# Performance work log

Measured on AMD Instinct MI355X. Metric: run time of the kernel, lower is better.

Reference implementation:

```python
import jax, jax.numpy as jnp
import numpy as np

N_NODES = 4096
N_EDGES = 524288
IN_DIM = 6
EMB_N = 4
EMB_D = 8
EDGE_D = 1
HID = 64
N_HEADS = 4
LN_EPS = 1e-5


def _layernorm(h, g, b):
    m = jnp.mean(h, axis=-1, keepdims=True)
    v = jnp.mean(jnp.square(h - m), axis=-1, keepdims=True)
    return (h - m) * jax.lax.rsqrt(v + LN_EPS) * g + b


def setup_inputs() -> dict:
    key = jax.random.key(0)
    ks = jax.random.split(key, 16)
    s = lambda fan_in: 1.0 / np.sqrt(fan_in)
    inp = {
        'x': jax.random.normal(ks[0], (N_NODES, IN_DIM), jnp.float32),
        'edge_attr': jax.random.uniform(ks[1], (N_EDGES, EDGE_D), jnp.float32),
        'entity_emb': jax.random.normal(ks[2], (EMB_N, EMB_D), jnp.float32),
        'lin1_w': jax.random.uniform(ks[3], (HID, IN_DIM + EMB_D + EDGE_D), jnp.float32, -s(15), s(15)),
        'lin1_b': jnp.zeros((HID,), jnp.float32),
        'lay_w': jax.random.uniform(ks[4], (HID, HID), jnp.float32, -s(HID), s(HID)),
        'lay_b': jnp.zeros((HID,), jnp.float32),
        'ln_g': jnp.ones((HID,), jnp.float32),
        'ln_b': jnp.zeros((HID,), jnp.float32),
        'in_proj_w': jax.random.uniform(ks[5], (3 * HID, HID), jnp.float32, -s(HID), s(HID)),
        'in_proj_b': jnp.zeros((3 * HID,), jnp.float32),
        'out_proj_w': jax.random.uniform(ks[6], (HID, HID), jnp.float32, -s(HID), s(HID)),
        'out_proj_b': jnp.zeros((HID,), jnp.float32),
        'an_g': jnp.ones((HID,), jnp.float32),
        'an_b': jnp.zeros((HID,), jnp.float32),
        'out_w': jax.random.uniform(ks[7], (HID, HID), jnp.float32, -s(HID), s(HID)),
        'out_b': jnp.zeros((HID,), jnp.float32),
        'edge_index': jax.random.randint(ks[8], (2, N_EDGES), 0, N_NODES, jnp.int64),
        'entity_type': jax.random.randint(ks[9], (N_NODES,), 0, EMB_N, jnp.int64),
    }
    return inp


def reference(x, edge_attr, entity_emb, lin1_w, lin1_b, lay_w, lay_b, ln_g, ln_b,
              in_proj_w, in_proj_b, out_proj_w, out_proj_b, an_g, an_b, out_w, out_b,
              edge_index, entity_type):
    # --- EmbedConv ---
    # concat node features with entity embedding: [N, 6+8]
    xe = jnp.concatenate([x, entity_emb[entity_type]], axis=-1)
    src, dst = edge_index[0], edge_index[1]
    # gather source nodes + edge attr: [E, 15]
    msg = jnp.concatenate([xe[src], edge_attr], axis=-1)
    msg = _layernorm(jax.nn.relu(msg @ lin1_w.T + lin1_b), ln_g, ln_b)
    # layer_N = 1 extra layer, shared LayerNorm
    msg = _layernorm(jax.nn.relu(msg @ lay_w.T + lay_b), ln_g, ln_b)
    # scatter-add aggregate into destination nodes: [N, 64]
    h = jax.ops.segment_sum(msg, dst, num_segments=N_NODES)
    # --- MultiheadAttention over all nodes as one sequence (eval: no dropout) ---
    qkv = h @ in_proj_w.T + in_proj_b  # [N, 3H]
    q, k, v = jnp.split(qkv, 3, axis=-1)
    hd = HID // N_HEADS
    q = q.reshape(N_NODES, N_HEADS, hd).transpose(1, 0, 2)  # [h, n, d]
    k = k.reshape(N_NODES, N_HEADS, hd).transpose(1, 0, 2)
    v = v.reshape(N_NODES, N_HEADS, hd).transpose(1, 0, 2)
    scores = jnp.einsum('hnd,hmd->hnm', q, k) / np.sqrt(hd)
    attn = jax.nn.softmax(scores, axis=-1)
    o = jnp.einsum('hnm,hmd->hnd', attn, v).transpose(1, 0, 2).reshape(N_NODES, HID)
    o = o @ out_proj_w.T + out_proj_b
    h = _layernorm(h + o, an_g, an_b)
    # --- output layer ---
    return h @ out_w.T + out_b
```

## Files before the change

### kernel.cpp

```cpp
#include <hip/hip_runtime.h>

#define N_NODES 4096
#define N_EDGES 524288
#define HID 64

typedef short short8 __attribute__((ext_vector_type(8)));
typedef float f32x4 __attribute__((ext_vector_type(4)));
typedef float f32x16 __attribute__((ext_vector_type(16)));

__device__ __forceinline__ float bcastf(float v, int l) {
    return __int_as_float(__builtin_amdgcn_readlane(__float_as_int(v), l));
}

__device__ __forceinline__ void wave_sum2(float& a, float& b) {
    #pragma unroll
    for (int off = 32; off > 0; off >>= 1) {
        a += __shfl_xor(a, off, 64);
        b += __shfl_xor(b, off, 64);
    }
}

__device__ __forceinline__ short f2bf(float f) {
    unsigned u = __float_as_uint(f);
    u = u + 0x7FFFu + ((u >> 16) & 1u);
    return (short)(u >> 16);
}
__device__ __forceinline__ float bf2f(short s) {
    return __uint_as_float(((unsigned)(unsigned short)s) << 16);
}
__device__ __forceinline__ void split_cheap(float f, short& hi, short& lo) {
    unsigned u = __float_as_uint(f);
    unsigned hb = u & 0xffff0000u;
    float lof = f - __uint_as_float(hb);
    hi = (short)(u >> 16);
    lo = (short)(__float_as_uint(lof) >> 16);
}

__global__ void hist_prep(const float* __restrict__ x, const float* __restrict__ emb,
                          const int* __restrict__ etype, const int* __restrict__ ei,
                          const float* __restrict__ w1, const float* __restrict__ b1,
                          const float* __restrict__ w2, const float* __restrict__ lng,
                          const float* __restrict__ lnb, const float* __restrict__ b2,
                          const float* __restrict__ ipw,
                          float* __restrict__ A1, int* __restrict__ cnt, int* __restrict__ rank,
                          unsigned short* __restrict__ w2fh, unsigned short* __restrict__ w2fl,
                          unsigned short* __restrict__ ipfh, unsigned short* __restrict__ ipfl,
                          float* __restrict__ b2p) {
    int tid = blockIdx.x * 256 + threadIdx.x;
    int d = ei[N_EDGES + tid];
    rank[tid] = atomicAdd(&cnt[d], 1);
    if (tid < N_NODES * 64) {
        int n = tid >> 6, f = tid & 63;
        const float* wr = w1 + f * 15;
        float acc = b1[f];
        #pragma unroll
        for (int k = 0; k < 6; k++) acc = fmaf(x[n * 6 + k], wr[k], acc);
        int e = etype[n];
        #pragma unroll
        for (int k = 0; k < 8; k++) acc = fmaf(emb[e * 8 + k], wr[6 + k], acc);
        A1[tid] = acc;
    }
    if (tid < 4096) {
        int idx = tid >> 9, ln = (tid >> 3) & 63, j = tid & 7;
        int mm = ln & 15, qq = ln >> 4;
        int g = idx >> 1, tt = idx & 1;
        int col = tt * 32 + qq * 8 + j;
        float w = w2[(g * 16 + mm) * 64 + col] * lng[col];
        short hi = f2bf(w);
        w2fh[tid] = (unsigned short)hi;
        w2fl[tid] = (unsigned short)f2bf(w - bf2f(hi));
    }
    if (tid < 12288) {
        int idx = tid >> 9, ln = (tid >> 3) & 63, j = tid & 7;
        int mm = ln & 15, qq = ln >> 4;
        int og = idx >> 1, tt = idx & 1;
        float w = ipw[(og * 16 + mm) * 64 + tt * 32 + qq * 8 + j];
        short hi = f2bf(w);
        ipfh[tid] = (unsigned short)hi;
        ipfl[tid] = (unsigned short)f2bf(w - bf2f(hi));
    }
    if (tid < 64) {
        float acc = b2[tid];
        for (int c = 0; c < 64; c++) acc = fmaf(w2[tid * 64 + c], lnb[c], acc);
        b2p[tid] = acc;
    }
}

__global__ void __launch_bounds__(256) scatter_scan(
        const int* __restrict__ cnt, const int* __restrict__ ei,
        const float* __restrict__ edge_attr, const int* __restrict__ rank,
        int* __restrict__ bnd,
        int* __restrict__ ssrc, float* __restrict__ sea) {
    __shared__ int lbnd[4096];
    __shared__ int wsum[4];
    int t = threadIdx.x;
    int base = t * 16;
    int v16[16];
    int T = 0;
    #pragma unroll
    for (int j = 0; j < 16; j++) { v16[j] = cnt[base + j]; T += v16[j]; }
    int inc = T;
    int l = t & 63;
    #pragma unroll
    for (int off = 1; off < 64; off <<= 1) {
        int v = __shfl_up(inc, off, 64);
        if (l >= off) inc += v;
    }
    if (l == 63) wsum[t >> 6] = inc;
    __syncthreads();
    int wo = 0;
    for (int w = 0; w < (t >> 6); w++) wo += wsum[w];
    int run = wo + inc - T;
    #pragma unroll
    for (int j = 0; j < 16; j++) {
        lbnd[base + j] = run;
        run += v16[j];
    }
    if (blockIdx.x == 0) {
        #pragma unroll
        for (int j = 0; j < 16; j++) bnd[base + j] = lbnd[base + j];
        if (t == 255) bnd[4096] = run;
    }
    __syncthreads();
    int e = blockIdx.x * 256 + t;
    int d = ei[N_EDGES + e];
    int pos = lbnd[d] + rank[e];
    ssrc[pos] = ei[e];
    sea[pos] = edge_attr[e];
}

__global__ void __launch_bounds__(256, 4) edge_gather_mfma(
        const float* __restrict__ A1,
        const int* __restrict__ ssrc, const float* __restrict__ sea,
        const int* __restrict__ bnd,
        const unsigned short* __restrict__ w2fh, const unsigned short* __restrict__ w2fl,
        const float* __restrict__ w1, const float* __restrict__ b2p,
        const float* __restrict__ lg, const float* __restrict__ lb,
        float* __restrict__ h) {
    __shared__ uint4 lw2h4[512];
    __shared__ uint4 lw2l4[512];
    __shared__ float hpart[4][64];
    int tid = threadIdx.x;
    {
        const uint4* gh = (const uint4*)w2fh;
        const uint4* gl = (const uint4*)w2fl;
        lw2h4[tid] = gh[tid];
        lw2h4[tid + 256] = gh[tid + 256];
        lw2l4[tid] = gl[tid];
        lw2l4[tid + 256] = gl[tid + 256];
    }
    const unsigned short* lw2h = (const unsigned short*)lw2h4;
    const unsigned short* lw2l = (const unsigned short*)lw2l4;

    int lane = tid & 63;
    int wv = tid >> 6;
    int m = lane & 15;
    int q = lane >> 4;

    float w14f[16];
    #pragma unroll
    for (int t2 = 0; t2 < 2; t2++)
        #pragma unroll
        for (int j = 0; j < 8; j++)
            w14f[t2 * 8 + j] = w1[(t2 * 32 + q * 8 + j) * 15 + 14];
    float b2v[4];
    #pragma unroll
    for (int g = 0; g < 4; g++) b2v[g] = b2p[g * 16 + m];

    int node = blockIdx.x;
    int start = bnd[node], end = bnd[node + 1];
    int ntiles = (end - start + 15) >> 4;
    float acc[4] = {0.f, 0.f, 0.f, 0.f};
    __syncthreads();

    for (int t = wv; t < ntiles; t += 4) {
        int base = start + t * 16;
        int e = base + m;
        int ec = (e < end) ? e : (end - 1);
        int srcn = ssrc[ec];
        float eav = sea[ec];
        const float* ar = A1 + srcn * 64 + q * 8;
        float4 va = *(const float4*)(ar);
        float4 vb = *(const float4*)(ar + 4);
        float4 vc = *(const float4*)(ar + 32);
        float4 vd = *(const float4*)(ar + 36);
        float v[16] = {va.x, va.y, va.z, va.w, vb.x, vb.y, vb.z, vb.w,
                       vc.x, vc.y, vc.z, vc.w, vd.x, vd.y, vd.z, vd.w};
        float s = 0.f, s2 = 0.f;
        #pragma unroll
        for (int j = 0; j < 16; j++) {
            float u = fmaxf(fmaf(w14f[j], eav, v[j]), 0.f);
            v[j] = u;
            s += u;
            s2 = fmaf(u, u, s2);
        }
        s += __shfl_xor(s, 16, 64);  s2 += __shfl_xor(s2, 16, 64);
        s += __shfl_xor(s, 32, 64);  s2 += __shfl_xor(s2, 32, 64);
        float mean = s * (1.f / 64.f);
        float var = s2 * (1.f / 64.f) - mean * mean;
        float rs = rsqrtf(var + 1e-5f);
        float a0 = -mean * rs;
        short8 a2h[2], a2l[2];
        #pragma unroll
        for (int t2 = 0; t2 < 2; t2++)
            #pragma unroll
            for (int j = 0; j < 8; j++) {
                short hi, lo;
                split_cheap(fmaf(v[t2 * 8 + j], rs, a0), hi, lo);
                a2h[t2][j] = hi;
                a2l[t2][j] = lo;
            }
        int ob = (t >> 20);
        float s_[4] = {0, 0, 0, 0}, s2_[4] = {0, 0, 0, 0};
        float t2v[4][4];
        #pragma unroll
        for (int g = 0; g < 4; g++) {
            f32x4 c = {0.f, 0.f, 0.f, 0.f};
            #pragma unroll
            for (int t2 = 0; t2 < 2; t2++) {
                short8 bh = *(const short8*)(lw2h + ((g * 2 + t2) * 64 + lane + ob) * 8);
                short8 bl = *(const short8*)(lw2l + ((g * 2 + t2) * 64 + lane + ob) * 8);
                c = __builtin_amdgcn_mfma_f32_16x16x32_bf16(a2l[t2], bh, c, 0, 0, 0);
                c = __builtin_amdgcn_mfma_f32_16x16x32_bf16(a2h[t2], bl, c, 0, 0, 0);
                c = __builtin_amdgcn_mfma_f32_16x16x32_bf16(a2h[t2], bh, c, 0, 0, 0);
            }
            #pragma unroll
            for (int i = 0; i < 4; i++) {
                float vv = fmaxf(c[i] + b2v[g], 0.f);
                t2v[g][i] = vv;
                s_[i] += vv;
                s2_[i] = fmaf(vv, vv, s2_[i]);
            }
        }
        #pragma unroll
        for (int off = 1; off < 16; off <<= 1)
            #pragma unroll
            for (int i = 0; i < 4; i++) {
                s_[i] += __shfl_xor(s_[i], off, 64);
                s2_[i] += __shfl_xor(s2_[i], off, 64);
            }
        #pragma unroll
        for (int i = 0; i < 4; i++) {
            float mean2 = s_[i] * (1.f / 64.f);
            float var2 = s2_[i] * (1.f / 64.f) - mean2 * mean2;
            float rs2 = rsqrtf(var2 + 1e-5f);
            bool valid = (base + q * 4 + i) < end;
            #pragma unroll
            for (int g = 0; g < 4; g++) {
                float z = (t2v[g][i] - mean2) * rs2;
                if (valid) acc[g] += z;
            }
        }
    }
    #pragma unroll
    for (int g = 0; g < 4; g++) {
        acc[g] += __shfl_xor(acc[g], 16, 64);
        acc[g] += __shfl_xor(acc[g], 32, 64);
    }
    float a01 = (q & 1) ? acc[1] : acc[0];
    float a23 = (q & 1) ? acc[3] : acc[2];
    float av = (q & 2) ? a23 : a01;
    hpart[wv][q * 16 + m] = av;
    __syncthreads();
    if (tid < 64) {
        float sum = hpart[0][tid] + hpart[1][tid] + hpart[2][tid] + hpart[3][tid];
        h[node * 64 + tid] = lg[tid] * sum + (float)(end - start) * lb[tid];
    }
}

__global__ void __launch_bounds__(256) qkv_mfma(
        const float* __restrict__ h, const float* __restrict__ b,
        const unsigned short* __restrict__ ipfh, const unsigned short* __restrict__ ipfl,
        unsigned short* __restrict__ qhp, unsigned short* __restrict__ qlp,
        unsigned short* __restrict__ khp, unsigned short* __restrict__ klp,
        unsigned short* __restrict__ vT) {
    int lane = threadIdx.x & 63;
    int wv = threadIdx.x >> 6;
    int m = lane & 15;
    int q = lane >> 4;
    int wid = blockIdx.x * 4 + wv;
    int tile = wid / 12;
    int og = wid - tile * 12;
    short8 bh[2], bl[2];
    #pragma unroll
    for (int t = 0; t < 2; t++) {
        bh[t] = *(const short8*)(ipfh + ((og * 2 + t) * 64 + lane) * 8);
        bl[t] = *(const short8*)(ipfl + ((og * 2 + t) * 64 + lane) * 8);
    }
    f32x4 c = {0.f, 0.f, 0.f, 0.f};
    #pragma unroll
    for (int t = 0; t < 2; t++) {
        const float* hr = h + (tile * 16 + m) * 64 + t * 32 + q * 8;
        float4 f0 = *(const float4*)hr;
        float4 f1 = *(const float4*)(hr + 4);
        float av8[8] = {f0.x, f0.y, f0.z, f0.w, f1.x, f1.y, f1.z, f1.w};
        short8 ah, al;
        #pragma unroll
        for (int j = 0; j < 8; j++) {
            short hi, lo;
            split_cheap(av8[j], hi, lo);
            ah[j] = hi;
            al[j] = lo;
        }
        c = __builtin_amdgcn_mfma_f32_16x16x32_bf16(al, bh[t], c, 0, 0, 0);
        c = __builtin_amdgcn_mfma_f32_16x16x32_bf16(ah, bl[t], c, 0, 0, 0);
        c = __builtin_amdgcn_mfma_f32_16x16x32_bf16(ah, bh[t], c, 0, 0, 0);
    }
    int o = og * 16 + m;
    float bias = b[o];
    #pragma unroll
    for (int r = 0; r < 4; r++) {
        int node = tile * 16 + q * 4 + r;
        float val = c[r] + bias;
        if (og < 4) {
            float aq = val * (0.25f * 1.44269504f);
            size_t idx = ((size_t)(og * N_NODES + node)) * 16 + m;
            short hi = f2bf(aq);
            qhp[idx] = (unsigned short)hi;
            qlp[idx] = (unsigned short)f2bf(aq - bf2f(hi));
        } else if (og < 8) {
            size_t idx = ((size_t)((og - 4) * N_NODES + node)) * 16 + m;
            short hi = f2bf(val);
            khp[idx] = (unsigned short)hi;
            klp[idx] = (unsigned short)f2bf(val - bf2f(hi));
        } else {
            int feat = (og - 8) * 16 + m;
            vT[(size_t)feat * N_NODES + node] = (unsigned short)f2bf(val);
        }
    }
}

__global__ void __launch_bounds__(256) attn_mfma(
        const unsigned short* __restrict__ qhp, const unsigned short* __restrict__ qlp,
        const unsigned short* __restrict__ khp, const unsigned short* __restrict__ klp,
        const unsigned short* __restrict__ vT,
        float* __restrict__ part_o, float* __restrict__ part_ml) {
    int lane = threadIdx.x & 63;
    int wv = threadIdx.x >> 6;
    int l31 = lane & 31;
    int hi = lane >> 5;
    const short8 vones = {0x3F80, 0x3F80, 0x3F80, 0x3F80, 0x3F80, 0x3F80, 0x3F80, 0x3F80};

    int wid = blockIdx.x * 4 + wv;
    int kc = wid & 7;
    int wqt = (wid >> 3) & 127;
    int head = wid >> 10;

    int qrow = wqt * 32 + l31;
    short8 aqh = *(const short8*)(qhp + ((size_t)(head * N_NODES + qrow)) * 16 + hi * 8);
    short8 aql = *(const short8*)(qlp + ((size_t)(head * N_NODES + qrow)) * 16 + hi * 8);

    const unsigned short* khb = khp + (size_t)head * N_NODES * 16;
    const unsigned short* klb = klp + (size_t)head * N_NODES * 16;
    const unsigned short* vtb = vT + (size_t)(head * 16 + (l31 & 15)) * N_NODES;

    float mS = -3e38f;
    f32x16 Ot = {0.f, 0.f, 0.f, 0.f, 0.f, 0.f, 0.f, 0.f,
                 0.f, 0.f, 0.f, 0.f, 0.f, 0.f, 0.f, 0.f};

    for (int bb = 0; bb < 16; bb++) {
        int n0 = kc * 512 + bb * 32;
        const unsigned short* kpb = khb + ((size_t)(n0 + l31)) * 16 + hi * 8;
        const unsigned short* kpl = klb + ((size_t)(n0 + l31)) * 16 + hi * 8;
        short8 bkh = *(const short8*)kpb;
        short8 bkl = *(const short8*)kpl;
        f32x16 S = {0.f, 0.f, 0.f, 0.f, 0.f, 0.f, 0.f, 0.f,
                    0.f, 0.f, 0.f, 0.f, 0.f, 0.f, 0.f, 0.f};
        S = __builtin_amdgcn_mfma_f32_32x32x16_bf16(bkh, aql, S, 0, 0, 0);
        S = __builtin_amdgcn_mfma_f32_32x32x16_bf16(bkl, aqh, S, 0, 0, 0);
        S = __builtin_amdgcn_mfma_f32_32x32x16_bf16(bkh, aqh, S, 0, 0, 0);
        float mr = S[0];
        #pragma unroll
        for (int r = 1; r < 16; r++) mr = fmaxf(mr, S[r]);
        mr = fmaxf(mr, __shfl_xor(mr, 32, 64));
        if (!__all(mr <= mS)) {
            float mn = fmaxf(mS, mr);
            float alpha = exp2f(mS - mn);
            mS = mn;
            #pragma unroll
            for (int r = 0; r < 9; r++) Ot[r] *= alpha;
        }
        float p[16];
        #pragma unroll
        for (int r = 0; r < 16; r++) p[r] = exp2f(S[r] - mS);
        unsigned w0, w1, w2, w3, u0, u1, u2, u3;
        asm("v_cvt_pk_bf16_f32 %0, %1, %2" : "=v"(w0) : "v"(p[0]), "v"(p[1]));
        asm("v_cvt_pk_bf16_f32 %0, %1, %2" : "=v"(w1) : "v"(p[2]), "v"(p[3]));
        asm("v_cvt_pk_bf16_f32 %0, %1, %2" : "=v"(w2) : "v"(p[4]), "v"(p[5]));
        asm("v_cvt_pk_bf16_f32 %0, %1, %2" : "=v"(w3) : "v"(p[6]), "v"(p[7]));
        asm("v_cvt_pk_bf16_f32 %0, %1, %2" : "=v"(u0) : "v"(p[8]), "v"(p[9]));
        asm("v_cvt_pk_bf16_f32 %0, %1, %2" : "=v"(u1) : "v"(p[10]), "v"(p[11]));
        asm("v_cvt_pk_bf16_f32 %0, %1, %2" : "=v"(u2) : "v"(p[12]), "v"(p[13]));
        asm("v_cvt_pk_bf16_f32 %0, %1, %2" : "=v"(u3) : "v"(p[14]), "v"(p[15]));
        asm("v_permlane32_swap_b32 %0, %1" : "+v"(w0), "+v"(w2));
        asm("v_permlane32_swap_b32 %0, %1" : "+v"(w1), "+v"(w3));
        asm("v_permlane32_swap_b32 %0, %1" : "+v"(u0), "+v"(u2));
        asm("v_permlane32_swap_b32 %0, %1" : "+v"(u1), "+v"(u3));
        union { unsigned u[4]; short8 s; } pf0, pf1;
        pf0.u[0] = w0; pf0.u[1] = w1; pf0.u[2] = w2; pf0.u[3] = w3;
        pf1.u[0] = u0; pf1.u[1] = u1; pf1.u[2] = u2; pf1.u[3] = u3;
        short8 v0, v1;
        if (l31 < 16) {
            v0 = *(const short8*)(vtb + n0 + hi * 8);
            v1 = *(const short8*)(vtb + n0 + 16 + hi * 8);
        } else if (l31 == 16) {
            v0 = vones; v1 = vones;
        } else {
            v0 = (short8)0; v1 = (short8)0;
        }
        Ot = __builtin_amdgcn_mfma_f32_32x32x16_bf16(v0, pf0.s, Ot, 0, 0, 0);
        Ot = __builtin_amdgcn_mfma_f32_32x32x16_bf16(v1, pf1.s, Ot, 0, 0, 0);
    }
    int qt16 = wqt * 2 + (l31 >> 4);
    int qi = l31 & 15;
    size_t pb = ((size_t)(head * 8 + kc) * 256 + qt16) * 256;
    f32x4 o0 = {Ot[0], Ot[1], Ot[2], Ot[3]};
    f32x4 o1 = {Ot[4], Ot[5], Ot[6], Ot[7]};
    *(f32x4*)(part_o + pb + qi * 16 + hi * 4) = o0;
    *(f32x4*)(part_o + pb + qi * 16 + 8 + hi * 4) = o1;
    if (lane < 32) {
        size_t mb = ((size_t)(head * 8 + kc) * 256 + qt16) * 32;
        part_ml[mb + qi] = mS;
        part_ml[mb + 16 + qi] = Ot[8];
    }
}

__global__ void post_kernel(const float* __restrict__ h,
                            const float* __restrict__ part_o, const float* __restrict__ part_ml,
                            const float* __restrict__ opw, const float* __restrict__ opb,
                            const float* __restrict__ ag, const float* __restrict__ ab,
                            const float* __restrict__ ow, const float* __restrict__ ob,
                            float* __restrict__ out) {
    __shared__ float wl1[64 * 65];
    __shared__ float wl2[64 * 65];
    for (int i = threadIdx.x; i < 4096; i += blockDim.x) {
        int r = i >> 6, c = i & 63;
        wl1[r * 65 + c] = opw[i];
        wl2[r * 65 + c] = ow[i];
    }
    __syncthreads();
    int lane = threadIdx.x & 63;
    int n = blockIdx.x * 4 + (threadIdx.x >> 6);
    int j = lane;
    int head = j >> 4, d = j & 15;
    int qt = n >> 4, qi = n & 15;
    float M = -3e38f, L = 0.f, Ov = 0.f;
    #pragma unroll
    for (int c = 0; c < 8; c++) {
        size_t base = ((size_t)(head * 8 + c) * 256 + qt);
        float mc = part_ml[base * 32 + qi];
        float lc = part_ml[base * 32 + 16 + qi];
        float ov = part_o[base * 256 + qi * 16 + d];
        if (mc > M) {
            float sc = exp2f(M - mc);
            M = mc;
            L = L * sc + lc;
            Ov = Ov * sc + ov;
        } else {
            float sc = exp2f(mc - M);
            L = fmaf(lc, sc, L);
            Ov = fmaf(ov, sc, Ov);
        }
    }
    float oj = Ov / L;
    float acc = opb[j];
    #pragma unroll
    for (int k = 0; k < 64; k++) acc = fmaf(wl1[j * 65 + k], bcastf(oj, k), acc);
    float r = h[n * 64 + j] + acc;
    float s = r, s2 = r * r;
    wave_sum2(s, s2);
    float mean = s * (1.f / 64.f);
    float var = s2 * (1.f / 64.f) - mean * mean;
    float hn = (r - mean) * rsqrtf(var + 1e-5f) * ag[j] + ab[j];
    float acc2 = ob[j];
    #pragma unroll
    for (int k = 0; k < 64; k++) acc2 = fmaf(wl2[j * 65 + k], bcastf(hn, k), acc2);
    out[n * 64 + j] = acc2;
}

extern "C" void kernel_launch(void* const* d_in, const int* in_sizes, int n_in,
                              void* d_out, int out_size, void* d_ws, size_t ws_size,
                              hipStream_t stream) {
    const float* x        = (const float*)d_in[0];
    const float* edge_attr= (const float*)d_in[1];
    const float* emb      = (const float*)d_in[2];
    const float* lin1_w   = (const float*)d_in[3];
    const float* lin1_b   = (const float*)d_in[4];
    const float* lay_w    = (const float*)d_in[5];
    const float* lay_b    = (const float*)d_in[6];
    const float* ln_g     = (const float*)d_in[7];
    const float* ln_b     = (const float*)d_in[8];
    const float* ipw      = (const float*)d_in[9];
    const float* ipb      = (const float*)d_in[10];
    const float* opw      = (const float*)d_in[11];
    const float* opb      = (const float*)d_in[12];
    const float* ang      = (const float*)d_in[13];
    const float* anb      = (const float*)d_in[14];
    const float* ow       = (const float*)d_in[15];
    const float* ob       = (const float*)d_in[16];
    const int*   ei       = (const int*)d_in[17];
    const int*   et       = (const int*)d_in[18];

    char* wsb = (char*)d_ws;
    size_t off = 0;
    float* A1             = (float*)(wsb + off);          off += 1048576;
    float* h              = (float*)(wsb + off);          off += 1048576;
    unsigned short* qhp   = (unsigned short*)(wsb + off); off += 524288;
    unsigned short* qlp   = (unsigned short*)(wsb + off); off += 524288;
    unsigned short* khp   = (unsigned short*)(wsb + off); off += 524288;
    unsigned short* klp   = (unsigned short*)(wsb + off); off += 524288;
    unsigned short* vT    = (unsigned short*)(wsb + off); off += 524288;
    float* part_o         = (float*)(wsb + off);          off += 8388608;
    float* part_ml        = (float*)(wsb + off);          off += 1048576;
    int*   cnt            = (int*)(wsb + off);            off += 16384;
    int*   bnd            = (int*)(wsb + off);            off += 16388;
    off = (off + 255) & ~(size_t)255;
    int*   rank           = (int*)(wsb + off);            off += 2097152;
    int*   ssrc           = (int*)(wsb + off);            off += 2097152;
    float* sea            = (float*)(wsb + off);          off += 2097152;
    unsigned short* w2fh  = (unsigned short*)(wsb + off); off += 8192;
    unsigned short* w2fl  = (unsigned short*)(wsb + off); off += 8192;
    unsigned short* ipfh  = (unsigned short*)(wsb + off); off += 24576;
    unsigned short* ipfl  = (unsigned short*)(wsb + off); off += 24576;
    float* b2p            = (float*)(wsb + off);          off += 256;

    (void)hipMemsetAsync(cnt, 0, 4096 * sizeof(int), stream);
    hist_prep<<<2048, 256, 0, stream>>>(x, emb, et, ei, lin1_w, lin1_b, lay_w, ln_g, ln_b,
                                        lay_b, ipw, A1, cnt, rank, w2fh, w2fl, ipfh, ipfl, b2p);
    scatter_scan<<<2048, 256, 0, stream>>>(cnt, ei, edge_attr, rank, bnd, ssrc, sea);
    edge_gather_mfma<<<4096, 256, 0, stream>>>(A1, ssrc, sea, bnd, w2fh, w2fl,
                                               lin1_w, b2p, ln_g, ln_b, h);
    qkv_mfma<<<768, 256, 0, stream>>>(h, ipb, ipfh, ipfl, qhp, qlp, khp, klp, vT);
    attn_mfma<<<1024, 256, 0, stream>>>(qhp, qlp, khp, klp, vT, part_o, part_ml);
    post_kernel<<<1024, 256, 0, stream>>>(h, part_o, part_ml, opw, opb, ang, anb, ow, ob,
                                          (float*)d_out);
}
```

Baseline: 227.2 us.

## Assign one node per wave in edge gather and prefetch next tiles

The edge gather kernel now gives each wave its own destination node (1024 blocks of 4 waves) instead of splitting one node's edges across four waves, which removes the shared-memory partial reduction and its barrier. It software-prefetches the next tile's source indices and edge attributes, and loads the w1 column 14 weights from a packed array prepared in hist_prep using vector loads. The attention kernel also prefetches the next K block's fragments before the current MFMAs. Per-node work is now serial within one wave, so imbalance in node degree and reduced parallelism per node may lengthen the tail.

```diff
diff --git a/kernel.cpp b/kernel.cpp
--- a/kernel.cpp
+++ b/kernel.cpp
@@ -45,7 +45,7 @@
                           float* __restrict__ A1, int* __restrict__ cnt, int* __restrict__ rank,
                           unsigned short* __restrict__ w2fh, unsigned short* __restrict__ w2fl,
                           unsigned short* __restrict__ ipfh, unsigned short* __restrict__ ipfl,
-                          float* __restrict__ b2p) {
+                          float* __restrict__ b2p, float* __restrict__ w14p) {
     int tid = blockIdx.x * 256 + threadIdx.x;
     int d = ei[N_EDGES + tid];
     rank[tid] = atomicAdd(&cnt[d], 1);
@@ -83,6 +83,7 @@
         float acc = b2[tid];
         for (int c = 0; c < 64; c++) acc = fmaf(w2[tid * 64 + c], lnb[c], acc);
         b2p[tid] = acc;
+        w14p[tid] = w1[tid * 15 + 14];
     }
 }
 
@@ -134,12 +135,11 @@
         const int* __restrict__ ssrc, const float* __restrict__ sea,
         const int* __restrict__ bnd,
         const unsigned short* __restrict__ w2fh, const unsigned short* __restrict__ w2fl,
-        const float* __restrict__ w1, const float* __restrict__ b2p,
+        const float* __restrict__ w14p, const float* __restrict__ b2p,
         const float* __restrict__ lg, const float* __restrict__ lb,
         float* __restrict__ h) {
     __shared__ uint4 lw2h4[512];
     __shared__ uint4 lw2l4[512];
-    __shared__ float hpart[4][64];
     int tid = threadIdx.x;
     {
         const uint4* gh = (const uint4*)w2fh;
@@ -158,32 +158,44 @@
     int q = lane >> 4;
 
     float w14f[16];
-    #pragma unroll
-    for (int t2 = 0; t2 < 2; t2++)
-        #pragma unroll
-        for (int j = 0; j < 8; j++)
-            w14f[t2 * 8 + j] = w1[(t2 * 32 + q * 8 + j) * 15 + 14];
+    {
+        float4 wa = *(const float4*)(w14p + q * 8);
+        float4 wb = *(const float4*)(w14p + q * 8 + 4);
+        float4 wc = *(const float4*)(w14p + 32 + q * 8);
+        float4 wd = *(const float4*)(w14p + 32 + q * 8 + 4);
+        w14f[0] = wa.x; w14f[1] = wa.y; w14f[2] = wa.z; w14f[3] = wa.w;
+        w14f[4] = wb.x; w14f[5] = wb.y; w14f[6] = wb.z; w14f[7] = wb.w;
+        w14f[8] = wc.x; w14f[9] = wc.y; w14f[10] = wc.z; w14f[11] = wc.w;
+        w14f[12] = wd.x; w14f[13] = wd.y; w14f[14] = wd.z; w14f[15] = wd.w;
+    }
     float b2v[4];
     #pragma unroll
     for (int g = 0; g < 4; g++) b2v[g] = b2p[g * 16 + m];
-
-    int node = blockIdx.x;
+    float lgv = lg[lane], lbv = lb[lane];
+
+    int node = blockIdx.x * 4 + wv;
     int start = bnd[node], end = bnd[node + 1];
     int ntiles = (end - start + 15) >> 4;
     float acc[4] = {0.f, 0.f, 0.f, 0.f};
     __syncthreads();
 
-    for (int t = wv; t < ntiles; t += 4) {
+    int srcn = 0; float eav = 0.f;
+    if (ntiles > 0) {
+        int ec = start + m; if (ec >= end) ec = end - 1;
+        srcn = ssrc[ec]; eav = sea[ec];
+    }
+    for (int t = 0; t < ntiles; t++) {
         int base = start + t * 16;
-        int e = base + m;
-        int ec = (e < end) ? e : (end - 1);
-        int srcn = ssrc[ec];
-        float eav = sea[ec];
         const float* ar = A1 + srcn * 64 + q * 8;
         float4 va = *(const float4*)(ar);
         float4 vb = *(const float4*)(ar + 4);
         float4 vc = *(const float4*)(ar + 32);
         float4 vd = *(const float4*)(ar + 36);
+        int srcn_n = srcn; float eav_n = eav;
+        if (t + 1 < ntiles) {
+            int e2 = base + 16 + m; if (e2 >= end) e2 = end - 1;
+            srcn_n = ssrc[e2]; eav_n = sea[e2];
+        }
         float v[16] = {va.x, va.y, va.z, va.w, vb.x, vb.y, vb.z, vb.w,
                        vc.x, vc.y, vc.z, vc.w, vd.x, vd.y, vd.z, vd.w};
         float s = 0.f, s2 = 0.f;
@@ -251,6 +263,7 @@
                 if (valid) acc[g] += z;
             }
         }
+        srcn = srcn_n; eav = eav_n;
     }
     #pragma unroll
     for (int g = 0; g < 4; g++) {
@@ -260,12 +273,7 @@
     float a01 = (q & 1) ? acc[1] : acc[0];
     float a23 = (q & 1) ? acc[3] : acc[2];
     float av = (q & 2) ? a23 : a01;
-    hpart[wv][q * 16 + m] = av;
-    __syncthreads();
-    if (tid < 64) {
-        float sum = hpart[0][tid] + hpart[1][tid] + hpart[2][tid] + hpart[3][tid];
-        h[node * 64 + tid] = lg[tid] * sum + (float)(end - start) * lb[tid];
-    }
+    h[node * 64 + lane] = lgv * av + (float)(end - start) * lbv;
 }
 
 __global__ void __launch_bounds__(256) qkv_mfma(
@@ -358,12 +366,16 @@
     f32x16 Ot = {0.f, 0.f, 0.f, 0.f, 0.f, 0.f, 0.f, 0.f,
                  0.f, 0.f, 0.f, 0.f, 0.f, 0.f, 0.f, 0.f};
 
+    size_t koff = ((size_t)(kc * 512 + l31)) * 16 + hi * 8;
+    short8 bkh = *(const short8*)(khb + koff);
+    short8 bkl = *(const short8*)(klb + koff);
+
     for (int bb = 0; bb < 16; bb++) {
         int n0 = kc * 512 + bb * 32;
-        const unsigned short* kpb = khb + ((size_t)(n0 + l31)) * 16 + hi * 8;
-        const unsigned short* kpl = klb + ((size_t)(n0 + l31)) * 16 + hi * 8;
-        short8 bkh = *(const short8*)kpb;
-        short8 bkl = *(const short8*)kpl;
+        int nbb = (bb + 1 < 16) ? (bb + 1) : 15;
+        size_t koffn = ((size_t)(kc * 512 + nbb * 32 + l31)) * 16 + hi * 8;
+        short8 nkh = *(const short8*)(khb + koffn);
+        short8 nkl = *(const short8*)(klb + koffn);
         f32x16 S = {0.f, 0.f, 0.f, 0.f, 0.f, 0.f, 0.f, 0.f,
                     0.f, 0.f, 0.f, 0.f, 0.f, 0.f, 0.f, 0.f};
         S = __builtin_amdgcn_mfma_f32_32x32x16_bf16(bkh, aql, S, 0, 0, 0);
@@ -410,6 +422,7 @@
         }
         Ot = __builtin_amdgcn_mfma_f32_32x32x16_bf16(v0, pf0.s, Ot, 0, 0, 0);
         Ot = __builtin_amdgcn_mfma_f32_32x32x16_bf16(v1, pf1.s, Ot, 0, 0, 0);
+        bkh = nkh; bkl = nkl;
     }
     int qt16 = wqt * 2 + (l31 >> 4);
     int qi = l31 & 15;
@@ -523,13 +536,15 @@
     unsigned short* ipfh  = (unsigned short*)(wsb + off); off += 24576;
     unsigned short* ipfl  = (unsigned short*)(wsb + off); off += 24576;
     float* b2p            = (float*)(wsb + off);          off += 256;
+    float* w14p           = (float*)(wsb + off);          off += 256;
 
     (void)hipMemsetAsync(cnt, 0, 4096 * sizeof(int), stream);
     hist_prep<<<2048, 256, 0, stream>>>(x, emb, et, ei, lin1_w, lin1_b, lay_w, ln_g, ln_b,
-                                        lay_b, ipw, A1, cnt, rank, w2fh, w2fl, ipfh, ipfl, b2p);
+                                        lay_b, ipw, A1, cnt, rank, w2fh, w2fl, ipfh, ipfl,
+                                        b2p, w14p);
     scatter_scan<<<2048, 256, 0, stream>>>(cnt, ei, edge_attr, rank, bnd, ssrc, sea);
-    edge_gather_mfma<<<4096, 256, 0, stream>>>(A1, ssrc, sea, bnd, w2fh, w2fl,
-                                               lin1_w, b2p, ln_g, ln_b, h);
+    edge_gather_mfma<<<1024, 256, 0, stream>>>(A1, ssrc, sea, bnd, w2fh, w2fl,
+                                               w14p, b2p, ln_g, ln_b, h);
     qkv_mfma<<<768, 256, 0, stream>>>(h, ipb, ipfh, ipfl, qhp, qlp, khp, klp, vT);
     attn_mfma<<<1024, 256, 0, stream>>>(qhp, qlp, khp, klp, vT, part_o, part_ml);
     post_kernel<<<1024, 256, 0, stream>>>(h, part_o, part_ml, opw, opb, ang, anb, ow, ob,
```

Result: no change. 224.7 us (-1.1%).
